# Kernel optimization log

Measured on AMD Instinct MI355X. Metric: run time of the kernel, lower is better.

Reference implementation:

```python
import jax, jax.numpy as jnp
import numpy as np

IN_FEAT = 66; D_MODEL = 512; KS = 10; DCT_N = 20; NUM_STAGE = 2; BN_EPS = 1e-5
HID = D_MODEL; GCN_IN = 2 * DCT_N


def get_dct_matrix(N):
    k = np.arange(N)[:, None]; i = np.arange(N)[None, :]
    w = np.full((N, 1), np.sqrt(2.0 / N)); w[0, 0] = np.sqrt(1.0 / N)
    dct = (w * np.cos(np.pi * (i + 0.5) * k / N)).astype(np.float32)
    idct = np.linalg.inv(dct).astype(np.float32)
    return jnp.asarray(dct), jnp.asarray(idct)


def conv1d(x, w):
    # x: [B, Cin, L], w: [Cout, Cin, K] -> [B, Cout, L-K+1]
    return jax.lax.conv_general_dilated(x, w, (1,), 'VALID', dimension_numbers=('NCH', 'OIH', 'NCH'))


def _forward(src, Wq1, Wq2, Wk1, Wk2, gc1_W, gc1_att, gc1_b, bn1_g, bn1_b,
             gcb_W, gcb_att, gcb_b, gcb_bn_g, gcb_bn_b, gc7_W, gc7_att, gc7_b,
             output_n, input_n):
    bs = src.shape[0]
    src = src[:, :input_n]                                  # [B, 50, F]
    vl = KS + output_n                                      # 35
    vn = input_n - KS - output_n + 1                        # 16
    dct_m, idct_m = get_dct_matrix(vl)

    key_in = jnp.swapaxes(src, 1, 2)[:, :, :input_n - output_n] / 1000.0   # [B, F, 25]
    query_in = jnp.swapaxes(src, 1, 2)[:, :, -KS:] / 1000.0                # [B, F, 10]

    # overlapping sliding windows -> per-window DCT coefficients
    idx = np.arange(vl)[None, :] + np.arange(vn)[:, None]   # [vn, vl]
    val = src[:, idx]                                       # [B, vn, vl, F]
    val = jnp.einsum('kv,bnvf->bnfk', dct_m[:DCT_N], val).reshape(bs, vn, IN_FEAT * DCT_N)

    key = jax.nn.relu(conv1d(jax.nn.relu(conv1d(key_in, Wk1)), Wk2))       # [B, D, vn]
    query = jax.nn.relu(conv1d(jax.nn.relu(conv1d(query_in, Wq1)), Wq2))   # [B, D, 1]

    score = jnp.einsum('bdq,bdn->bqn', query, key) + 1e-15                 # [B, 1, vn]
    att = score / jnp.sum(score, axis=2, keepdims=True)                    # sum-normalized attention
    dct_att = jnp.einsum('bqn,bnf->bqf', att, val)[:, 0].reshape(bs, IN_FEAT, DCT_N)

    # last KS frames + last frame repeated output_n times
    idx2 = np.concatenate([np.arange(input_n - KS, input_n), np.full(output_n, input_n - 1)])
    input_gcn = src[:, idx2]                                               # [B, vl, F]
    dct_in = jnp.swapaxes(jnp.einsum('kv,bvf->bkf', dct_m[:DCT_N], input_gcn), 1, 2)  # [B, F, DCT_N]
    x = jnp.concatenate([dct_in, dct_att], axis=-1)                        # [B, F, 2*DCT_N]

    # ---- GCN (eval mode: dropout off, BN with fresh running stats mean=0, var=1) ----
    def gc(y, W, A, bias):
        return jnp.einsum('nm,bmf->bnf', A, y @ W) + bias

    def bn(y, g, be):
        b_, n_, f_ = y.shape
        v = y.reshape(b_, n_ * f_)
        v = v * (g / np.float32(np.sqrt(1.0 + BN_EPS))) + be
        return v.reshape(b_, n_, f_)

    y = jnp.tanh(bn(gc(x, gc1_W, gc1_att, gc1_b), bn1_g, bn1_b))
    for st in range(NUM_STAGE):
        y0 = y
        y = jnp.tanh(bn(gc(y, gcb_W[st, 0], gcb_att[st, 0], gcb_b[st, 0]), gcb_bn_g[st, 0], gcb_bn_b[st, 0]))
        y = jnp.tanh(bn(gc(y, gcb_W[st, 1], gcb_att[st, 1], gcb_b[st, 1]), gcb_bn_g[st, 1], gcb_bn_b[st, 1]))
        y = y + y0
    dct_out = gc(y, gc7_W, gc7_att, gc7_b) + x                             # [B, F, 2*DCT_N]

    out = jnp.einsum('vk,bfk->bvf', idct_m[:, :DCT_N], dct_out[:, :, :DCT_N])  # [B, vl, F]
    return out[:, :, None, :]                                              # [B, vl, itera=1, F]


def setup_inputs():
    key = jax.random.key(0)
    ks = jax.random.split(key, 11)
    bs = 512; s = 0.05; f32 = jnp.float32
    return {
        'src': jax.random.normal(ks[0], (bs, 50, IN_FEAT), f32),
        'Wq1': jax.random.normal(ks[1], (D_MODEL, IN_FEAT, 6), f32) * s,
        'Wq2': jax.random.normal(ks[2], (D_MODEL, D_MODEL, 5), f32) * s,
        'Wk1': jax.random.normal(ks[3], (D_MODEL, IN_FEAT, 6), f32) * s,
        'Wk2': jax.random.normal(ks[4], (D_MODEL, D_MODEL, 5), f32) * s,
        'gc1_W': jax.random.normal(ks[5], (GCN_IN, HID), f32) * s,
        'gc1_att': jax.random.normal(ks[6], (IN_FEAT, IN_FEAT), f32) * s,
        'gc1_b': jnp.zeros((HID,), f32),
        'bn1_g': jnp.ones((IN_FEAT * HID,), f32),
        'bn1_b': jnp.zeros((IN_FEAT * HID,), f32),
        'gcb_W': jax.random.normal(ks[7], (NUM_STAGE, 2, HID, HID), f32) * s,
        'gcb_att': jax.random.normal(ks[8], (NUM_STAGE, 2, IN_FEAT, IN_FEAT), f32) * s,
        'gcb_b': jnp.zeros((NUM_STAGE, 2, HID), f32),
        'gcb_bn_g': jnp.ones((NUM_STAGE, 2, IN_FEAT * HID), f32),
        'gcb_bn_b': jnp.zeros((NUM_STAGE, 2, IN_FEAT * HID), f32),
        'gc7_W': jax.random.normal(ks[9], (HID, GCN_IN), f32) * s,
        'gc7_att': jax.random.normal(ks[10], (IN_FEAT, IN_FEAT), f32) * s,
        'gc7_b': jnp.zeros((GCN_IN,), f32),
        'output_n': 25,
        'input_n': 50,
    }


def reference(src, Wq1, Wq2, Wk1, Wk2, gc1_W, gc1_att, gc1_b, bn1_g, bn1_b,
              gcb_W, gcb_att, gcb_b, gcb_bn_g, gcb_bn_b, gc7_W, gc7_att, gc7_b,
              output_n, input_n):
    return _forward(src, Wq1, Wq2, Wk1, Wk2, gc1_W, gc1_att, gc1_b, bn1_g, bn1_b,
                    gcb_W, gcb_att, gcb_b, gcb_bn_g, gcb_bn_b, gc7_W, gc7_att, gc7_b,
                    output_n, input_n)
```

## Files before the change

### kernel.cpp

```cpp
#include <hip/hip_runtime.h>
#include <math.h>

#define PI_D 3.14159265358979323846

#define BSZ   512
#define NODE  66
#define VL    35
#define DCTN  20

static constexpr float BN_INVS = 0.99999500003749969f;

typedef unsigned short u16;
typedef unsigned int   u32;
using bf16x8 = __attribute__((ext_vector_type(8))) short;
using f32x4  = __attribute__((ext_vector_type(4))) float;

#define AS1 __attribute__((address_space(1)))
#define AS3 __attribute__((address_space(3)))

__device__ __forceinline__ void gl16(const u16* g, u16* l) {
    __builtin_amdgcn_global_load_lds((const AS1 u32*)g, (AS3 u32*)l, 16, 0, 0);
}

__device__ inline u16 f2bf(float f) {
    union { float f; u32 u; } v; v.f = f;
    u32 r = v.u + 0x7FFFu + ((v.u >> 16) & 1u);
    return (u16)(r >> 16);
}
__device__ inline float bf2f(u16 b) {
    union { u32 u; float f; } v; v.u = ((u32)b) << 16;
    return v.f;
}

__global__ void dct_kernel(float* __restrict__ dct20) {
    int i = blockIdx.x * blockDim.x + threadIdx.x;
    if (i < DCTN * VL) {
        int k = i / VL, v = i - k * VL;
        double w = (k == 0) ? sqrt(1.0 / VL) : sqrt(2.0 / VL);
        dct20[i] = (float)(w * cos(PI_D * (v + 0.5) * k / (double)VL));
    }
}

__global__ void cvt_gcb(const float* __restrict__ W, u16* __restrict__ Wt) {
    int l = blockIdx.y;
    int i = blockIdx.x * 256 + threadIdx.x;
    int n = i >> 9, k = i & 511;
    Wt[(size_t)l * 262144 + i] = f2bf(W[(size_t)l * 262144 + (size_t)k * 512 + n]);
}
__global__ void cvt_gc1(const float* __restrict__ W, u16* __restrict__ Wt) {
    int i = blockIdx.x * 256 + threadIdx.x;
    int n = i >> 6, k = i & 63;
    Wt[i] = (k < 40) ? f2bf(W[k * 512 + n]) : (u16)0;
}
__global__ void cvt_gc7(const float* __restrict__ W, u16* __restrict__ Wt) {
    int i = blockIdx.x * 256 + threadIdx.x;
    int n = i >> 9, k = i & 511;
    Wt[i] = (n < 20) ? f2bf(W[k * 40 + n]) : (u16)0;
}
__global__ void cvt_w1(const float* __restrict__ W, u16* __restrict__ Wt) {
    int i = blockIdx.x * 256 + threadIdx.x;
    int d = i / 416, k = i - d * 416;
    float v = 0.f;
    if (k < 396) { int h = k / 66, c = k - h * 66; v = W[d * 396 + c * 6 + h]; }
    Wt[i] = f2bf(v);
}
__global__ void cvt_w2(const float* __restrict__ W, u16* __restrict__ Wt) {
    int i = blockIdx.x * 256 + threadIdx.x;
    int d = i / 2560, k = i - d * 2560;
    int h = k >> 9, c = k & 511;
    Wt[i] = f2bf(W[(size_t)d * 2560 + c * 5 + h]);
}
__global__ void cvt_att(const float* __restrict__ gc1A, const float* __restrict__ gcbA,
                        const float* __restrict__ gc7A, u16* __restrict__ Abf) {
    int l = blockIdx.y;
    int i = blockIdx.x * 256 + threadIdx.x;
    if (i < 8320) {
        int r = i / 104, c = i - (i / 104) * 104;
        float v = 0.f;
        if (r < 66 && c < 66) {
            const float* A = (l == 0) ? gc1A : (l <= 4 ? gcbA + (size_t)(l - 1) * 4356 : gc7A);
            v = A[r * 66 + c];
        }
        Abf[(size_t)l * 8320 + i] = f2bf(v);
    }
}

template<int EPI>
__global__ __launch_bounds__(256) void gc_fused(const u16* __restrict__ Y,
                                                const u16* __restrict__ Wt,
                                                const u16* __restrict__ Ab,
                                                void* __restrict__ Yout, int K,
                                                const float* __restrict__ bias,
                                                const float* __restrict__ g,
                                                const float* __restrict__ be,
                                                const u16* __restrict__ yres,
                                                const float* __restrict__ xres) {
    __shared__ u16 smem[19624];
    u16* AsF = smem;
    u16* BsF = smem + 4608;
    u16* zT  = smem;

    const int tid = threadIdx.x;
    const int b0 = blockIdx.x * 2;
    const int n0 = blockIdx.y * 128;
    const int lane = tid & 63, w = tid >> 6;
    const int row16 = lane & 15, grp = lane >> 4;

    int k0;
    auto stageA = [&](int c) {
        int flat = c * 1024 + lane * 16;
        int plane = flat / 2304;
        int row = (flat - plane * 2304) >> 4;
        long grow = (long)b0 * 66 + row; if (grow > 33791) grow = 33791;
        gl16(Y + (size_t)grow * K + k0 + plane * 8, AsF + c * 512);
    };
    auto stageB = [&](int c) {
        int row = ((c & 1) << 6) + lane;
        gl16(Wt + (size_t)(n0 + row) * K + k0 + (c >> 1) * 8, BsF + c * 512);
    };

    f32x4 acc[9][2] = {};
    for (k0 = 0; k0 < K; k0 += 32) {
        stageA(w); stageA(w + 4); if (w == 0) stageA(8);
        stageB(2 * w); stageB(2 * w + 1);
        __syncthreads();
        const int aoff = grp * 1152 + row16 * 8;
        const int boff = grp * 1024 + (w * 32 + row16) * 8;
        bf16x8 b[2];
#pragma unroll
        for (int nt = 0; nt < 2; ++nt) b[nt] = *(const bf16x8*)&BsF[boff + nt * 128];
#pragma unroll
        for (int mc = 0; mc < 3; ++mc) {
            bf16x8 a[3];
#pragma unroll
            for (int i = 0; i < 3; ++i) a[i] = *(const bf16x8*)&AsF[aoff + (mc * 3 + i) * 128];
#pragma unroll
            for (int i = 0; i < 3; ++i)
#pragma unroll
                for (int nt = 0; nt < 2; ++nt)
                    acc[mc * 3 + i][nt] = __builtin_amdgcn_mfma_f32_16x16x32_bf16(a[i], b[nt], acc[mc * 3 + i][nt], 0, 0, 0);
        }
        __syncthreads();
    }

    for (int i = tid; i < 128 * 20; i += 256) {
        int f = i / 20, j = i - (i / 20) * 20;
        int c = (j < 6) ? (66 + j) : (132 + j);
        zT[f * 152 + c] = 0;
    }
    for (int i = tid; i < 168; i += 256) zT[19456 + i] = 0;

#pragma unroll
    for (int mt = 0; mt < 9; ++mt) {
        int m = mt * 16 + grp * 4;
        if (m < 132) {
#pragma unroll
            for (int nt = 0; nt < 2; ++nt) {
                int f = w * 32 + nt * 16 + row16;
                u16 e0 = f2bf(acc[mt][nt][0]), e1 = f2bf(acc[mt][nt][1]);
                u16 e2 = f2bf(acc[mt][nt][2]), e3 = f2bf(acc[mt][nt][3]);
                if (m + 3 < 66 || m >= 66) {
                    int col = (m < 66) ? m : m + 6;
                    *(u32*)&zT[f * 152 + col]     = (u32)e0 | ((u32)e1 << 16);
                    *(u32*)&zT[f * 152 + col + 2] = (u32)e2 | ((u32)e3 << 16);
                } else {
                    zT[f * 152 + 64] = e0; zT[f * 152 + 65] = e1;
                    zT[f * 152 + 72] = e2; zT[f * 152 + 73] = e3;
                }
            }
        }
    }

    bf16x8 aA[5][3];
#pragma unroll
    for (int mt = 0; mt < 5; ++mt)
#pragma unroll
        for (int k2 = 0; k2 < 3; ++k2)
            aA[mt][k2] = *(const bf16x8*)&Ab[(mt * 16 + row16) * 104 + k2 * 32 + grp * 8];
    __syncthreads();

    f32x4 acc2[2][5][2] = {};
#pragma unroll
    for (int bb = 0; bb < 2; ++bb) {
        const int base = bb * 72;
#pragma unroll
        for (int k2 = 0; k2 < 3; ++k2) {
            bf16x8 bz[2];
#pragma unroll
            for (int ft = 0; ft < 2; ++ft)
                bz[ft] = *(const bf16x8*)&zT[(w * 32 + ft * 16 + row16) * 152 + base + k2 * 32 + grp * 8];
#pragma unroll
            for (int mt = 0; mt < 5; ++mt)
#pragma unroll
                for (int ft = 0; ft < 2; ++ft)
                    acc2[bb][mt][ft] = __builtin_amdgcn_mfma_f32_16x16x32_bf16(aA[mt][k2], bz[ft], acc2[bb][mt][ft], 0, 0, 0);
        }
    }

#pragma unroll
    for (int bb = 0; bb < 2; ++bb) {
        const int bidx = b0 + bb;
#pragma unroll
        for (int mt = 0; mt < 5; ++mt) {
            int nb = mt * 16 + grp * 4;
#pragma unroll
            for (int ft = 0; ft < 2; ++ft) {
                int c = n0 + w * 32 + ft * 16 + row16;
#pragma unroll
                for (int j = 0; j < 4; ++j) {
                    int n = nb + j;
                    if (n < 66) {
                        float v = acc2[bb][mt][ft][j];
                        if constexpr (EPI == 4) {
                            if (c < 20)
                                ((float*)Yout)[(size_t)bidx * 1320 + n * 20 + c] =
                                    v + bias[c] + xres[(size_t)bidx * 2640 + n * 40 + c];
                        } else {
                            int gi = n * 512 + c;
                            float z = v + bias[c];
                            float t = tanhf(z * (g[gi] * BN_INVS) + be[gi]);
                            if constexpr (EPI == 3) t += bf2f(yres[((size_t)bidx * 66 + n) * 512 + c]);
                            ((u16*)Yout)[((size_t)bidx * 66 + n) * 512 + c] = f2bf(t);
                        }
                    }
                }
            }
        }
    }
}

template<int ASRC, int EPI, int TOUT, int TIN, int T0>
__global__ __launch_bounds__(256) void gemm_uni(const void* __restrict__ Asrc,
                                                const u16* __restrict__ Bt,
                                                void* __restrict__ Cout,
                                                int M, int K, int Nvalid, int ldc) {
    __shared__ u16 AsF[4096];
    __shared__ u16 BsF[4096];
    const int tid = threadIdx.x;
    const int r0 = blockIdx.x * 128, n0 = blockIdx.y * 128;
    const int lane = tid & 63, w = tid >> 6;
    const int wr = (w >> 1) * 64, wc = (w & 1) * 64;
    const int row16 = lane & 15, grp = lane >> 4;
    const int sr = tid >> 1, sq = (tid & 1) * 16;

    const float* apf = nullptr;
    if constexpr (ASRC == 2) {
        int R = r0 + sr; int b = R / TOUT, t = R - b * TOUT;
        apf = (const float*)Asrc + (size_t)b * 3300 + (T0 + t) * 66 + sq;
    }

    f32x4 acc[4][4] = {};
    for (int k0 = 0; k0 < K; k0 += 32) {
        if constexpr (ASRC == 1) {
#pragma unroll
            for (int i = 0; i < 2; ++i) {
                int c = 2 * w + i;
                int row = ((c & 1) << 6) + lane;
                int R = r0 + row; int b = R / TOUT, t = R - b * TOUT;
                gl16((const u16*)Asrc + ((size_t)b * TIN + t) * 512 + k0 + (c >> 1) * 8,
                     AsF + c * 512);
            }
        } else {
#pragma unroll
            for (int j = 0; j < 16; ++j) {
                int k = k0 + sq + j;
                float vin = 0.f;
                if (k < 396) vin = apf[k0 + j];
                int col = sq + j;
                AsF[(col >> 3) * 1024 + sr * 8 + (col & 7)] = f2bf(vin * 1e-3f);
            }
        }
#pragma unroll
        for (int i = 0; i < 2; ++i) {
            int c = 2 * w + i;
            int row = ((c & 1) << 6) + lane;
            gl16(Bt + (size_t)(n0 + row) * K + k0 + (c >> 1) * 8, BsF + c * 512);
        }
        __syncthreads();
        bf16x8 a[4], b[4];
#pragma unroll
        for (int m = 0; m < 4; ++m) a[m] = *(const bf16x8*)&AsF[grp * 1024 + (wr + m * 16 + row16) * 8];
#pragma unroll
        for (int n = 0; n < 4; ++n) b[n] = *(const bf16x8*)&BsF[grp * 1024 + (wc + n * 16 + row16) * 8];
#pragma unroll
        for (int m = 0; m < 4; ++m)
#pragma unroll
            for (int n = 0; n < 4; ++n)
                acc[m][n] = __builtin_amdgcn_mfma_f32_16x16x32_bf16(a[m], b[n], acc[m][n], 0, 0, 0);
        __syncthreads();
    }
#pragma unroll
    for (int m = 0; m < 4; ++m) {
        int rb = r0 + wr + m * 16 + grp * 4;
#pragma unroll
        for (int n = 0; n < 4; ++n) {
            int c = n0 + wc + n * 16 + row16;
            if (c < Nvalid) {
#pragma unroll
                for (int j = 0; j < 4; ++j) {
                    float v = fmaxf(acc[m][n][j], 0.f);
                    if constexpr (EPI == 0) ((u16*)Cout)[(size_t)(rb + j) * ldc + c] = f2bf(v);
                    else                    ((float*)Cout)[(size_t)(rb + j) * ldc + c] = v;
                }
            }
        }
    }
}

__global__ __launch_bounds__(256) void att_kernel(const float* __restrict__ qT,
                                                  const float* __restrict__ kT,
                                                  float* __restrict__ att) {
    const int b = blockIdx.x, tid = threadIdx.x;
    __shared__ float part[256];
    __shared__ float sc[16];
    int n = tid >> 4, j = tid & 15;
    const float* q = qT + b * 512;
    const float* k = kT + b * 8192 + n * 512;
    float acc = 0.f;
    for (int d = j; d < 512; d += 16) acc += q[d] * k[d];
    part[tid] = acc;
    __syncthreads();
    if (tid < 16) {
        float s = 0.f;
        for (int jj = 0; jj < 16; ++jj) s += part[tid * 16 + jj];
        sc[tid] = s + 1e-15f;
    }
    __syncthreads();
    if (tid == 0) {
        float tot = 0.f;
        for (int nn = 0; nn < 16; ++nn) tot += sc[nn];
        float inv = 1.f / tot;
        for (int nn = 0; nn < 16; ++nn) att[b * 16 + nn] = sc[nn] * inv;
    }
}

__global__ __launch_bounds__(256) void xbuild(const float* __restrict__ src,
                                              const float* __restrict__ att,
                                              const float* __restrict__ dct20,
                                              float* __restrict__ x,
                                              u16* __restrict__ xbf) {
    const int b = blockIdx.x, tid = threadIdx.x;
    __shared__ float s_src[50 * 66];
    __shared__ float s_sacc[VL * 66];
    __shared__ float s_d[DCTN * VL];
    __shared__ float s_att[16];
    for (int i = tid; i < 3300; i += 256) s_src[i] = src[b * 3300 + i];
    for (int i = tid; i < DCTN * VL; i += 256) s_d[i] = dct20[i];
    if (tid < 16) s_att[tid] = att[b * 16 + tid];
    __syncthreads();
    for (int i = tid; i < VL * 66; i += 256) {
        int v = i / 66, f = i - (i / 66) * 66;
        float a = 0.f;
#pragma unroll
        for (int n = 0; n < 16; ++n) a += s_att[n] * s_src[(n + v) * 66 + f];
        s_sacc[i] = a;
    }
    __syncthreads();
    for (int i = tid; i < 66 * DCTN; i += 256) {
        int f = i / DCTN, kq = i - (i / DCTN) * DCTN;
        float din = 0.f, datt = 0.f;
        for (int v = 0; v < VL; ++v) {
            float dv = s_d[kq * VL + v];
            int t2 = (v < 10) ? (40 + v) : 49;
            din += dv * s_src[t2 * 66 + f];
            datt += dv * s_sacc[v * 66 + f];
        }
        x[b * 2640 + f * 40 + kq] = din;
        x[b * 2640 + f * 40 + 20 + kq] = datt;
        xbf[(size_t)b * 4224 + f * 64 + kq] = f2bf(din);
        xbf[(size_t)b * 4224 + f * 64 + 20 + kq] = f2bf(datt);
    }
    for (int i = tid; i < 66 * 24; i += 256) {
        int f = i / 24, kp = 40 + (i - (i / 24) * 24);
        xbf[(size_t)b * 4224 + f * 64 + kp] = 0;
    }
}

__global__ __launch_bounds__(256) void final_out(const float* __restrict__ dctout,
                                                 const float* __restrict__ dct20,
                                                 float* __restrict__ out) {
    const int b = blockIdx.x, tid = threadIdx.x;
    __shared__ float ds[DCTN * VL];
    __shared__ float dos[66 * 20];
    for (int i = tid; i < DCTN * VL; i += 256) ds[i] = dct20[i];
    for (int i = tid; i < 1320; i += 256) dos[i] = dctout[(size_t)b * 1320 + i];
    __syncthreads();
    for (int o = tid; o < VL * 66; o += 256) {
        int v = o / 66, f = o - (o / 66) * 66;
        float acc = 0.f;
#pragma unroll
        for (int k = 0; k < DCTN; ++k) acc += ds[k * VL + v] * dos[f * 20 + k];
        out[(size_t)b * 2310 + o] = acc;
    }
}

extern "C" void kernel_launch(void* const* d_in, const int* in_sizes, int n_in,
                              void* d_out, int out_size, void* d_ws, size_t ws_size,
                              hipStream_t stream) {
    const float* src     = (const float*)d_in[0];
    const float* Wq1     = (const float*)d_in[1];
    const float* Wq2     = (const float*)d_in[2];
    const float* Wk1     = (const float*)d_in[3];
    const float* Wk2     = (const float*)d_in[4];
    const float* gc1_W   = (const float*)d_in[5];
    const float* gc1_att = (const float*)d_in[6];
    const float* gc1_b   = (const float*)d_in[7];
    const float* bn1_g   = (const float*)d_in[8];
    const float* bn1_b   = (const float*)d_in[9];
    const float* gcb_W   = (const float*)d_in[10];
    const float* gcb_att = (const float*)d_in[11];
    const float* gcb_b   = (const float*)d_in[12];
    const float* gcb_g   = (const float*)d_in[13];
    const float* gcb_be  = (const float*)d_in[14];
    const float* gc7_W   = (const float*)d_in[15];
    const float* gc7_att = (const float*)d_in[16];
    const float* gc7_b   = (const float*)d_in[17];
    float* out = (float*)d_out;

    unsigned char* base = (unsigned char*)d_ws;
    size_t off = 0;
    auto take = [&](size_t bytes) -> void* {
        void* p = base + off;
        off += (bytes + 255) & ~(size_t)255;
        return p;
    };
    u16*   yA     = (u16*)take((size_t)33792 * 512 * 2);
    u16*   yB     = (u16*)take((size_t)33792 * 512 * 2);
    float* xb     = (float*)take((size_t)512 * 2640 * 4);
    u16*   xbf    = (u16*)take((size_t)512 * 4224 * 2);
    float* dct20  = (float*)take(2800);
    float* dctout = (float*)take((size_t)512 * 1320 * 4);
    u16*   key1   = (u16*)take((size_t)512 * 20 * 512 * 2);
    u16*   q1     = (u16*)take((size_t)512 * 5 * 512 * 2);
    float* keyT   = (float*)take((size_t)8192 * 512 * 4);
    float* queryT = (float*)take((size_t)512 * 512 * 4);
    float* attw   = (float*)take((size_t)512 * 16 * 4);
    u16*   WtGcb  = (u16*)take((size_t)4 * 512 * 512 * 2);
    u16*   WtGc1  = (u16*)take((size_t)512 * 64 * 2);
    u16*   WtGc7  = (u16*)take((size_t)128 * 512 * 2);
    u16*   WtW1k  = (u16*)take((size_t)512 * 416 * 2);
    u16*   WtW1q  = (u16*)take((size_t)512 * 416 * 2);
    u16*   WtW2k  = (u16*)take((size_t)512 * 2560 * 2);
    u16*   WtW2q  = (u16*)take((size_t)512 * 2560 * 2);
    u16*   Abf    = (u16*)take((size_t)6 * 8320 * 2);

    dct_kernel<<<2, 384, 0, stream>>>(dct20);
    cvt_att<<<dim3(33, 6), 256, 0, stream>>>(gc1_att, gcb_att, gc7_att, Abf);
    cvt_gcb<<<dim3(1024, 4), 256, 0, stream>>>(gcb_W, WtGcb);
    cvt_gc1<<<128, 256, 0, stream>>>(gc1_W, WtGc1);
    cvt_gc7<<<256, 256, 0, stream>>>(gc7_W, WtGc7);
    cvt_w1<<<832, 256, 0, stream>>>(Wk1, WtW1k);
    cvt_w1<<<832, 256, 0, stream>>>(Wq1, WtW1q);
    cvt_w2<<<5120, 256, 0, stream>>>(Wk2, WtW2k);
    cvt_w2<<<5120, 256, 0, stream>>>(Wq2, WtW2q);

    gemm_uni<2, 0, 20, 25, 0><<<dim3(80, 4), 256, 0, stream>>>(
        src, WtW1k, key1, 10240, 416, 512, 512);
    gemm_uni<2, 0, 5, 10, 40><<<dim3(20, 4), 256, 0, stream>>>(
        src, WtW1q, q1, 2560, 416, 512, 512);
    gemm_uni<1, 1, 16, 20, 0><<<dim3(64, 4), 256, 0, stream>>>(
        key1, WtW2k, keyT, 8192, 2560, 512, 512);
    gemm_uni<1, 1, 1, 5, 0><<<dim3(4, 4), 256, 0, stream>>>(
        q1, WtW2q, queryT, 512, 2560, 512, 512);
    att_kernel<<<BSZ, 256, 0, stream>>>(queryT, keyT, attw);
    xbuild<<<BSZ, 256, 0, stream>>>(src, attw, dct20, xb, xbf);

    gc_fused<2><<<dim3(256, 4), 256, 0, stream>>>(
        xbf, WtGc1, Abf, yA, 64, gc1_b, bn1_g, bn1_b, nullptr, nullptr);

    for (int st = 0; st < 2; ++st) {
        const u16* W0 = WtGcb + (size_t)(st * 2 + 0) * 262144;
        const u16* W1 = WtGcb + (size_t)(st * 2 + 1) * 262144;
        const u16* A0 = Abf + (size_t)(1 + st * 2) * 8320;
        const u16* A1 = Abf + (size_t)(2 + st * 2) * 8320;
        const float* b0  = gcb_b + (size_t)(st * 2 + 0) * 512;
        const float* b1  = gcb_b + (size_t)(st * 2 + 1) * 512;
        const float* g0  = gcb_g + (size_t)(st * 2 + 0) * 33792;
        const float* g1  = gcb_g + (size_t)(st * 2 + 1) * 33792;
        const float* be0 = gcb_be + (size_t)(st * 2 + 0) * 33792;
        const float* be1 = gcb_be + (size_t)(st * 2 + 1) * 33792;
        gc_fused<2><<<dim3(256, 4), 256, 0, stream>>>(
            yA, W0, A0, yB, 512, b0, g0, be0, nullptr, nullptr);
        gc_fused<3><<<dim3(256, 4), 256, 0, stream>>>(
            yB, W1, A1, yA, 512, b1, g1, be1, yA, nullptr);
    }

    gc_fused<4><<<dim3(256, 1), 256, 0, stream>>>(
        yA, WtGc7, Abf + (size_t)5 * 8320, dctout, 512, gc7_b, nullptr, nullptr, nullptr, xb);
    final_out<<<BSZ, 256, 0, stream>>>(dctout, dct20, out);
}
```

Measured before the change: 830.7 us.

## Double-buffer LDS tiles in gc_fused and gemm_uni K-loops

Splits shared memory into two stage buffers in both GEMM kernels. The next K-slice is prefetched into one buffer while MFMAs run on the other, which removes one barrier per iteration and overlaps global-to-LDS loads with compute. gemm_uni's LDS footprint doubles, which may lower occupancy. gc_fused fits both buffers inside its existing shared array.

```diff
diff --git a/kernel.cpp b/kernel.cpp
--- a/kernel.cpp
+++ b/kernel.cpp
@@ -96,9 +96,7 @@
                                                 const u16* __restrict__ yres,
                                                 const float* __restrict__ xres) {
     __shared__ u16 smem[19624];
-    u16* AsF = smem;
-    u16* BsF = smem + 4608;
-    u16* zT  = smem;
+    u16* zT = smem;
 
     const int tid = threadIdx.x;
     const int b0 = blockIdx.x * 2;
@@ -106,24 +104,50 @@
     const int lane = tid & 63, w = tid >> 6;
     const int row16 = lane & 15, grp = lane >> 4;
 
-    int k0;
-    auto stageA = [&](int c) {
-        int flat = c * 1024 + lane * 16;
-        int plane = flat / 2304;
-        int row = (flat - plane * 2304) >> 4;
-        long grow = (long)b0 * 66 + row; if (grow > 33791) grow = 33791;
-        gl16(Y + (size_t)grow * K + k0 + plane * 8, AsF + c * 512);
+    auto stage = [&](int buf, int k0) {
+        u16* A = smem + buf * 8704;
+        u16* B = A + 4608;
+        {
+            int c = w;
+            int flat = c * 1024 + lane * 16;
+            int plane = flat / 2304;
+            int row = (flat - plane * 2304) >> 4;
+            long grow = (long)b0 * 66 + row; if (grow > 33791) grow = 33791;
+            gl16(Y + (size_t)grow * K + k0 + plane * 8, A + c * 512);
+        }
+        {
+            int c = w + 4;
+            int flat = c * 1024 + lane * 16;
+            int plane = flat / 2304;
+            int row = (flat - plane * 2304) >> 4;
+            long grow = (long)b0 * 66 + row; if (grow > 33791) grow = 33791;
+            gl16(Y + (size_t)grow * K + k0 + plane * 8, A + c * 512);
+        }
+        if (w == 0) {
+            int c = 8;
+            int flat = c * 1024 + lane * 16;
+            int plane = flat / 2304;
+            int row = (flat - plane * 2304) >> 4;
+            long grow = (long)b0 * 66 + row; if (grow > 33791) grow = 33791;
+            gl16(Y + (size_t)grow * K + k0 + plane * 8, A + c * 512);
+        }
+#pragma unroll
+        for (int i = 0; i < 2; ++i) {
+            int c = 2 * w + i;
+            int row = ((c & 1) << 6) + lane;
+            gl16(Wt + (size_t)(n0 + row) * K + k0 + (c >> 1) * 8, B + c * 512);
+        }
     };
-    auto stageB = [&](int c) {
-        int row = ((c & 1) << 6) + lane;
-        gl16(Wt + (size_t)(n0 + row) * K + k0 + (c >> 1) * 8, BsF + c * 512);
-    };
+
+    stage(0, 0);
+    __syncthreads();
 
     f32x4 acc[9][2] = {};
-    for (k0 = 0; k0 < K; k0 += 32) {
-        stageA(w); stageA(w + 4); if (w == 0) stageA(8);
-        stageB(2 * w); stageB(2 * w + 1);
-        __syncthreads();
+    int cur = 0;
+    for (int k0 = 0; k0 < K; k0 += 32) {
+        if (k0 + 32 < K) stage(cur ^ 1, k0 + 32);
+        const u16* AsF = smem + cur * 8704;
+        const u16* BsF = AsF + 4608;
         const int aoff = grp * 1152 + row16 * 8;
         const int boff = grp * 1024 + (w * 32 + row16) * 8;
         bf16x8 b[2];
@@ -141,6 +165,7 @@
                     acc[mc * 3 + i][nt] = __builtin_amdgcn_mfma_f32_16x16x32_bf16(a[i], b[nt], acc[mc * 3 + i][nt], 0, 0, 0);
         }
         __syncthreads();
+        cur ^= 1;
     }
 
     for (int i = tid; i < 128 * 20; i += 256) {
@@ -234,8 +259,7 @@
                                                 const u16* __restrict__ Bt,
                                                 void* __restrict__ Cout,
                                                 int M, int K, int Nvalid, int ldc) {
-    __shared__ u16 AsF[4096];
-    __shared__ u16 BsF[4096];
+    __shared__ u16 smem[16384];
     const int tid = threadIdx.x;
     const int r0 = blockIdx.x * 128, n0 = blockIdx.y * 128;
     const int lane = tid & 63, w = tid >> 6;
@@ -249,8 +273,9 @@
         apf = (const float*)Asrc + (size_t)b * 3300 + (T0 + t) * 66 + sq;
     }
 
-    f32x4 acc[4][4] = {};
-    for (int k0 = 0; k0 < K; k0 += 32) {
+    auto stage = [&](int buf, int k0) {
+        u16* A = smem + buf * 8192;
+        u16* B = A + 4096;
         if constexpr (ASRC == 1) {
 #pragma unroll
             for (int i = 0; i < 2; ++i) {
@@ -258,7 +283,7 @@
                 int row = ((c & 1) << 6) + lane;
                 int R = r0 + row; int b = R / TOUT, t = R - b * TOUT;
                 gl16((const u16*)Asrc + ((size_t)b * TIN + t) * 512 + k0 + (c >> 1) * 8,
-                     AsF + c * 512);
+                     A + c * 512);
             }
         } else {
 #pragma unroll
@@ -267,16 +292,26 @@
                 float vin = 0.f;
                 if (k < 396) vin = apf[k0 + j];
                 int col = sq + j;
-                AsF[(col >> 3) * 1024 + sr * 8 + (col & 7)] = f2bf(vin * 1e-3f);
+                A[(col >> 3) * 1024 + sr * 8 + (col & 7)] = f2bf(vin * 1e-3f);
             }
         }
 #pragma unroll
         for (int i = 0; i < 2; ++i) {
             int c = 2 * w + i;
             int row = ((c & 1) << 6) + lane;
-            gl16(Bt + (size_t)(n0 + row) * K + k0 + (c >> 1) * 8, BsF + c * 512);
-        }
-        __syncthreads();
+            gl16(Bt + (size_t)(n0 + row) * K + k0 + (c >> 1) * 8, B + c * 512);
+        }
+    };
+
+    stage(0, 0);
+    __syncthreads();
+
+    f32x4 acc[4][4] = {};
+    int cur = 0;
+    for (int k0 = 0; k0 < K; k0 += 32) {
+        if (k0 + 32 < K) stage(cur ^ 1, k0 + 32);
+        const u16* AsF = smem + cur * 8192;
+        const u16* BsF = AsF + 4096;
         bf16x8 a[4], b[4];
 #pragma unroll
         for (int m = 0; m < 4; ++m) a[m] = *(const bf16x8*)&AsF[grp * 1024 + (wr + m * 16 + row16) * 8];
@@ -288,6 +323,7 @@
             for (int n = 0; n < 4; ++n)
                 acc[m][n] = __builtin_amdgcn_mfma_f32_16x16x32_bf16(a[m], b[n], acc[m][n], 0, 0, 0);
         __syncthreads();
+        cur ^= 1;
     }
 #pragma unroll
     for (int m = 0; m < 4; ++m) {
```

Measured after the change: 769.6 us. -7.4%, faster.
